# Kernel optimization log

Hardware: AMD Instinct MI355X
Metric: run time of the kernel (lower is better)

The kernel has to match this reference:

```python
import jax, jax.numpy as jnp
import numpy as np

B, T, D, H, K = 8, 512, 768, 8, 4
HD = D // H
SCALE = 1.0 / float(np.sqrt(HD))
EPS = 1e-5


def _ln(x, g, b):
    m = jnp.mean(x, -1, keepdims=True)
    v = jnp.mean((x - m) ** 2, -1, keepdims=True)
    return (x - m) * jax.lax.rsqrt(v + EPS) * g + b


def _attn(q, k, v, mask=None):
    # q,k,v: [B,T,D] -> multi-head scaled dot product, returns [B,T,D]
    sp = lambda t: t.reshape(B, T, H, HD).transpose(0, 2, 1, 3)  # [B,H,T,hd]
    a = jnp.einsum('bhqd,bhkd->bhqk', sp(q), sp(k)) * SCALE
    if mask is not None:
        a = jnp.where(mask, -jnp.inf, a)
    a = jax.nn.softmax(a, -1)
    o = jnp.einsum('bhqk,bhkd->bhqd', a, sp(v))
    return o.transpose(0, 2, 1, 3).reshape(B, T, D)


def setup_inputs() -> dict:
    key = jax.random.key(0)
    ks = iter(jax.random.split(key, 20))
    n = lambda shp: jax.random.normal(next(ks), shp, jnp.float32) * 0.02
    z = lambda shp: jnp.zeros(shp, jnp.float32)
    o = lambda shp: jnp.ones(shp, jnp.float32)
    return dict(
        x=jax.random.normal(next(ks), (B, T, D), jnp.float32),
        router_w1=n((128, D)), router_b1=z((128,)),
        router_w2=n((2 * K, 128)), router_b2=z((2 * K,)),
        norm_s_g=o((D,)), norm_s_b=z((D,)),
        norm_t_g=o((D,)), norm_t_b=z((D,)),
        norm_mlp_g=o((D,)), norm_mlp_b=z((D,)),
        sp_wqkv=n((K, 3 * D, D)), sp_bqkv=z((K, 3 * D)),
        sp_wo=n((K, D, D)), sp_bo=z((K, D)),
        tp_wq=n((K, D, D)), tp_bq=z((K, D)),
        tp_wk=n((K, D, D)), tp_bk=z((K, D)),
        tp_wv=n((K, D, D)), tp_bv=z((K, D)),
        tp_wo=n((K, D, D)), tp_bo=z((K, D)),
        cross_wqkv=n((3 * D, D)), cross_bqkv=z((3 * D,)),
        cross_wo=n((D, D)), cross_bo=z((D,)),
        mlp_w1=n((4 * D, D)), mlp_b1=z((4 * D,)),
        mlp_w2=n((D, 4 * D)), mlp_b2=z((D,)),
    )


def _forward(x, router_w1, router_b1, router_w2, router_b2,
             norm_s_g, norm_s_b, norm_t_g, norm_t_b, norm_mlp_g, norm_mlp_b,
             sp_wqkv, sp_bqkv, sp_wo, sp_bo,
             tp_wq, tp_bq, tp_wk, tp_bk, tp_wv, tp_bv, tp_wo, tp_bo,
             cross_wqkv, cross_bqkv, cross_wo, cross_bo,
             mlp_w1, mlp_b1, mlp_w2, mlp_b2):
    # --- router: top-1 expert per sample for each branch ---
    h = jax.nn.gelu(x.mean(1) @ router_w1.T + router_b1, approximate=False)
    route = jax.nn.softmax(h @ router_w2.T + router_b2, -1)  # [B, 2K]
    idx_s = jnp.argmax(route[:, :K], -1)  # [B] top-1 spatial expert
    idx_t = jnp.argmax(route[:, K:], -1)  # [B] top-1 temporal expert

    # --- spatial branch: per-sample routed MultiheadAttention (self-attn) ---
    xn = _ln(x, norm_s_g, norm_s_b)
    qkv = jnp.einsum('btd,bed->bte', xn, sp_wqkv[idx_s]) + sp_bqkv[idx_s][:, None, :]
    q, k, v = jnp.split(qkv, 3, -1)
    so = _attn(q, k, v)
    spatial_out = jnp.einsum('btd,bed->bte', so, sp_wo[idx_s]) + sp_bo[idx_s][:, None, :]

    # --- temporal branch: per-sample routed causal attention (with residual) ---
    xt = _ln(x, norm_t_g, norm_t_b)
    qt = jnp.einsum('btd,bed->bte', xt, tp_wq[idx_t]) + tp_bq[idx_t][:, None, :]
    kt = jnp.einsum('btd,bed->bte', xt, tp_wk[idx_t]) + tp_bk[idx_t][:, None, :]
    vt = jnp.einsum('btd,bed->bte', xt, tp_wv[idx_t]) + tp_bv[idx_t][:, None, :]
    causal = jnp.triu(jnp.ones((T, T), bool), 1)
    to = _attn(qt, kt, vt, mask=causal)
    to = jnp.einsum('btd,bed->bte', to, tp_wo[idx_t]) + tp_bo[idx_t][:, None, :]
    temporal_out = xt + to  # CausalTimeAttention2 adds residual to its (normed) query

    # --- cross attention fusing the two branches ---
    cq = spatial_out @ cross_wqkv[:D].T + cross_bqkv[:D]
    ck = temporal_out @ cross_wqkv[D:2 * D].T + cross_bqkv[D:2 * D]
    cv = temporal_out @ cross_wqkv[2 * D:].T + cross_bqkv[2 * D:]
    fused = _attn(cq, ck, cv) @ cross_wo.T + cross_bo

    x = x + fused
    y = jax.nn.gelu(_ln(x, norm_mlp_g, norm_mlp_b) @ mlp_w1.T + mlp_b1, approximate=False)
    x = x + (y @ mlp_w2.T + mlp_b2)
    return x


def reference(x, router_w1, router_b1, router_w2, router_b2,
              norm_s_g, norm_s_b, norm_t_g, norm_t_b, norm_mlp_g, norm_mlp_b,
              sp_wqkv, sp_bqkv, sp_wo, sp_bo,
              tp_wq, tp_bq, tp_wk, tp_bk, tp_wv, tp_bv, tp_wo, tp_bo,
              cross_wqkv, cross_bqkv, cross_wo, cross_bo,
              mlp_w1, mlp_b1, mlp_w2, mlp_b2):
    return _forward(x, router_w1, router_b1, router_w2, router_b2,
                    norm_s_g, norm_s_b, norm_t_g, norm_t_b, norm_mlp_g, norm_mlp_b,
                    sp_wqkv, sp_bqkv, sp_wo, sp_bo,
                    tp_wq, tp_bq, tp_wk, tp_bk, tp_wv, tp_bv, tp_wo, tp_bo,
                    cross_wqkv, cross_bqkv, cross_wo, cross_bo,
                    mlp_w1, mlp_b1, mlp_w2, mlp_b2)
```

## Files before the change

### kernel.cpp

```cpp
#include <hip/hip_runtime.h>
#include <math.h>

#define BB 8
#define TT 512
#define DD 768
#define HH 8
#define HDIM 96
#define DDDD 589824LL

typedef short s16x8 __attribute__((ext_vector_type(8)));
typedef float f32x4 __attribute__((ext_vector_type(4)));
typedef unsigned short u16;

__device__ inline unsigned short f2bf(float f) {
    union { float f; unsigned u; } v; v.f = f;
    unsigned u = v.u;
    unsigned r = (u + 0x7fffu + ((u >> 16) & 1u)) >> 16;
    return (unsigned short)r;
}

__device__ inline float bf2f(u16 h) {
    union { unsigned u; float f; } v; v.u = ((unsigned)h) << 16; return v.f;
}

__device__ inline float gelu_exact(float x) {
    return 0.5f * x * (1.0f + erff(x * 0.70710678118654752440f));
}

__device__ __forceinline__ void gload16(const void* g, void* l) {
    __builtin_amdgcn_global_load_lds(
        (const __attribute__((address_space(1))) unsigned int*)g,
        (__attribute__((address_space(3))) unsigned int*)l,
        16, 0, 0);
}

__device__ __forceinline__ long long tix(int m, int k, int ldn) {
    return ((long long)(m >> 6) * (ldn >> 3) + (k >> 3)) * 512 + ((m & 63) << 3) + (k & 7);
}

#define CUM1  7077888LL
#define CUM2  9437184LL
#define CUM5  16515072LL
#define CUM6  18874368LL
#define CUM7  20643840LL
#define CUM8  21233664LL
#define CUM9  23592960LL
#define CUM10 25952256LL

__global__ __launch_bounds__(256) void cvt_kernel(
    const float* __restrict__ s0, const float* __restrict__ s1,
    const float* __restrict__ s2, const float* __restrict__ s3,
    const float* __restrict__ s4, const float* __restrict__ s5,
    const float* __restrict__ s6, const float* __restrict__ s7,
    const float* __restrict__ s8, const float* __restrict__ s9,
    u16* __restrict__ dpool)
{
    int t = blockIdx.x;
    const float* sa = nullptr; const float* sb = nullptr; const float* sc = nullptr;
    long long dbase; int K = 768; int tpmode = 0;
    if (t < 864) {
        int e = t / 216; t -= e * 216;
        sa = s0 + (long long)e * 2304 * 768; dbase = e * 3 * DDDD;
    } else if (t < 1152) {
        t -= 864; int e = t / 72; t -= e * 72;
        sa = s1 + (long long)e * DDDD; dbase = CUM1 + e * DDDD;
    } else if (t < 2016) {
        t -= 1152; int e = t / 216; t -= e * 216; tpmode = 1;
        sa = s2 + (long long)e * DDDD; sb = s3 + (long long)e * DDDD;
        sc = s4 + (long long)e * DDDD; dbase = CUM2 + e * 3 * DDDD;
    } else if (t < 2304) {
        t -= 2016; int e = t / 72; t -= e * 72;
        sa = s5 + (long long)e * DDDD; dbase = CUM5 + e * DDDD;
    } else if (t < 2520) {
        t -= 2304; sa = s6; dbase = CUM6;
    } else if (t < 2592) {
        t -= 2520; sa = s7; dbase = CUM7;
    } else if (t < 2880) {
        t -= 2592; sa = s8; dbase = CUM8;
    } else {
        t -= 2880; sa = s9; dbase = CUM9; K = 3072;
    }
    int tiles_k = K >> 6;
    int nt = t / tiles_k, kb = t - nt * tiles_k;
    int n0 = nt * 128, k0 = kb * 64;

    __shared__ u16 lds[8256];

    int tid = threadIdx.x;
    #pragma unroll
    for (int it = 0; it < 4; ++it) {
        int sl = tid + it * 256;
        int r = sl >> 3, kw = sl & 7;
        int n = n0 + r;
        const float* src;
        if (tpmode) {
            if (n < 768)       src = sa + (long long)n * 768;
            else if (n < 1536) src = sb + (long long)(n - 768) * 768;
            else               src = sc + (long long)(n - 1536) * 768;
            src += k0 + kw * 8;
        } else {
            src = sa + (long long)n * K + k0 + kw * 8;
        }
        float4 a = *(const float4*)src;
        float4 b = *(const float4*)(src + 4);
        s16x8 o;
        o[0] = f2bf(a.x); o[1] = f2bf(a.y); o[2] = f2bf(a.z); o[3] = f2bf(a.w);
        o[4] = f2bf(b.x); o[5] = f2bf(b.y); o[6] = f2bf(b.z); o[7] = f2bf(b.w);
        *(s16x8*)&lds[(kw * 129 + r) * 8] = o;
    }
    __syncthreads();
    long long dbase2 = dbase + ((long long)nt * (K >> 3) + (long long)kb * 8) * 1024;
    #pragma unroll
    for (int it = 0; it < 4; ++it) {
        int sl = tid + it * 256;
        int kw = sl >> 7, r = sl & 127;
        *(s16x8*)(dpool + dbase2 + (long long)sl * 8) = *(const s16x8*)&lds[(kw * 129 + r) * 8];
    }
}

__global__ __launch_bounds__(256) void pack_tpb_kernel(
    const float* __restrict__ bq, const float* __restrict__ bk,
    const float* __restrict__ bv, float* __restrict__ dst)
{
    int t = blockIdx.x * 256 + threadIdx.x;
    if (t >= 4 * 2304) return;
    int e = t / 2304, n = t - e * 2304;
    float v = (n < 768) ? bq[e * 768 + n]
            : (n < 1536) ? bk[e * 768 + n - 768]
            : bv[e * 768 + n - 1536];
    dst[t] = v;
}

#define SLABB 4096

template<int OUT_MODE, int RES_MODE>
__global__ __launch_bounds__(256) void gemm_bf16_kernel(
    const u16* __restrict__ A, long long sAb,
    const u16* __restrict__ B, const int* __restrict__ bidx, long long sBexp,
    void* __restrict__ Cv, long long sCb, int ldc,
    const float* __restrict__ bias, long long sBiasExp,
    const void* __restrict__ residv, long long sResB, int ldr,
    int act, int N, int K)
{
    int nbx = gridDim.x, nby = gridDim.y;
    int nblk = nbx * nby * (int)gridDim.z;
    int lin = blockIdx.x + nbx * (blockIdx.y + nby * blockIdx.z);
    int q = nblk >> 3, r = nblk & 7;
    int xcd = lin & 7, pos = lin >> 3;
    int nl = (xcd < r ? xcd * (q + 1) : r * (q + 1) + (xcd - r) * q) + pos;
    int bx = nl % nbx; int t1 = nl / nbx; int by = t1 % nby; int bz = t1 / nby;

    int zb = bz;
    int kw8 = K >> 3;
    const u16* Ab = A + zb * sAb + (long long)by * kw8 * 512;
    const u16* Bb = B + (bidx ? (long long)bidx[zb] * sBexp : 0)
                      + (long long)bx * kw8 * 1024;
    const float* biasb = bias ? (bias + (bidx ? (long long)bidx[zb] * sBiasExp : 0)) : nullptr;

    __shared__ __align__(16) u16 Bs[6][SLABB];

    int tid = threadIdx.x;
    int wave = tid >> 6, lane = tid & 63;
    int wr = wave >> 1, wc = wave & 1;
    int lrow = lane & 15, lkg = lane >> 4;

    f32x4 acc[2][4];
    #pragma unroll
    for (int i = 0; i < 2; i++)
        #pragma unroll
        for (int j = 0; j < 4; j++)
            acc[i][j] = (f32x4){0.f, 0.f, 0.f, 0.f};

    long long aoff0 = (long long)lkg * 512 + (wr * 32 + 0 * 16 + lrow) * 8;
    long long aoff1 = (long long)lkg * 512 + (wr * 32 + 1 * 16 + lrow) * 8;

    const u16* bgt = Bb + tid * 8;
    u16* bl0 = (u16*)Bs + tid * 8;
    u16* bl1 = (u16*)Bs + (tid + 256) * 8;

    s16x8 abuf[3][2];

    int nK = K >> 5;

    gload16(bgt,            bl0);
    gload16(bgt + 2048,     bl1);
    gload16(bgt + SLABB,        bl0 + SLABB);
    gload16(bgt + SLABB + 2048, bl1 + SLABB);
    gload16(bgt + 2 * SLABB,        bl0 + 2 * SLABB);
    gload16(bgt + 2 * SLABB + 2048, bl1 + 2 * SLABB);
    abuf[0][0] = *(const s16x8*)(Ab + aoff0);
    abuf[0][1] = *(const s16x8*)(Ab + aoff1);
    gload16(bgt + 3 * SLABB,        bl0 + 3 * SLABB);
    gload16(bgt + 3 * SLABB + 2048, bl1 + 3 * SLABB);
    abuf[1][0] = *(const s16x8*)(Ab + 2048 + aoff0);
    abuf[1][1] = *(const s16x8*)(Ab + 2048 + aoff1);
    gload16(bgt + 4 * SLABB,        bl0 + 4 * SLABB);
    gload16(bgt + 4 * SLABB + 2048, bl1 + 4 * SLABB);

    for (int ktb = 0; ktb < nK; ktb += 6) {
        #pragma unroll
        for (int u = 0; u < 6; ++u) {
            int kt = ktb + u;
            if (kt + 6 <= nK) asm volatile("s_waitcnt vmcnt(6)" ::: "memory");
            else              asm volatile("s_waitcnt vmcnt(0)" ::: "memory");
            __builtin_amdgcn_s_barrier();
            __builtin_amdgcn_sched_barrier(0);

            if (kt + 2 < nK) {
                const u16* ap = Ab + (long long)(kt + 2) * 2048;
                abuf[(u + 2) % 3][0] = *(const s16x8*)(ap + aoff0);
                abuf[(u + 2) % 3][1] = *(const s16x8*)(ap + aoff1);
            }
            if (kt + 5 < nK) {
                const u16* bp = bgt + (long long)(kt + 5) * SLABB;
                int sl = (u + 5) % 6;
                gload16(bp,        bl0 + sl * SLABB);
                gload16(bp + 2048, bl1 + sl * SLABB);
            }

            const u16* Bsb = &Bs[u][0];
            s16x8 bf[4];
            #pragma unroll
            for (int j = 0; j < 4; ++j)
                bf[j] = *(const s16x8*)&Bsb[(lkg * 128 + wc * 64 + j * 16 + lrow) * 8];
            #pragma unroll
            for (int i = 0; i < 2; ++i)
                #pragma unroll
                for (int j = 0; j < 4; ++j)
                    acc[i][j] = __builtin_amdgcn_mfma_f32_16x16x32_bf16(abuf[u % 3][i], bf[j], acc[i][j], 0, 0, 0);
        }
    }

    int n0 = bx * 128;
    int m0 = by * 64;
    float* Cf = (float*)Cv + zb * sCb;
    u16* Ch = (u16*)Cv + zb * sCb;
    const float* Rf = (const float*)residv + zb * sResB;
    const u16* Rh = (const u16*)residv + zb * sResB;
    int col16 = lane & 15;
    int rq = (lane >> 4) * 4;
    #pragma unroll
    for (int j = 0; j < 4; ++j) {
        int n = n0 + wc * 64 + j * 16 + col16;
        float bv = biasb ? biasb[n] : 0.0f;
        #pragma unroll
        for (int i = 0; i < 2; ++i) {
            #pragma unroll
            for (int r2 = 0; r2 < 4; ++r2) {
                int m = m0 + wr * 32 + i * 16 + rq + r2;
                float v = acc[i][j][r2] + bv;
                if (act == 1) v = gelu_exact(v);
                if (RES_MODE == 1) v += Rf[(long long)m * ldr + n];
                if (RES_MODE == 2) v += bf2f(Rh[tix(m, n, ldr)]);
                if (OUT_MODE == 0) Cf[(long long)m * ldc + n] = v;
                if (OUT_MODE == 1) Ch[(long long)m * ldc + n] = f2bf(v);
                if (OUT_MODE == 2) Ch[tix(m, n, ldc)] = f2bf(v);
            }
        }
    }
}

__global__ __launch_bounds__(256, 2) void attn_kernel(
    const u16* __restrict__ QKV, u16* __restrict__ Out,
    int causal, float scale)
{
    int qt = blockIdx.x;
    int bh = blockIdx.y;
    int b = bh >> 3;
    int h = bh & 7;
    const u16* Qb = QKV + (long long)b * TT * 3 * DD + (long long)h * HDIM;
    const u16* Kb = Qb + DD;
    const u16* Vb = Qb + 2 * DD;
    u16* Ob = Out + (long long)b * TT * DD;

    __shared__ __align__(16) u16 Qs[64 * 104];
    __shared__ __align__(16) u16 Ks[64 * 104];
    __shared__ __align__(16) u16 Vs[96 * 72];
    __shared__ __align__(16) u16 Ps[64 * 72];

    int tid = threadIdx.x;
    int wave = tid >> 6;
    int lane = tid & 63;
    int col16 = lane & 15;
    int lkg = lane >> 4;
    int lk = lkg * 8;
    int m0 = qt * 64;

    #pragma unroll
    for (int it = 0; it < 3; ++it) {
        int s = tid + it * 256;
        int r = s / 12, c8 = (s % 12) * 8;
        *(s16x8*)&Qs[r * 104 + c8] = *(const s16x8*)(Qb + (long long)(m0 + r) * (3 * DD) + c8);
    }
    __syncthreads();

    s16x8 qf[3];
    #pragma unroll
    for (int kk = 0; kk < 3; ++kk)
        qf[kk] = *(const s16x8*)&Qs[(wave * 16 + col16) * 104 + kk * 32 + lk];

    f32x4 acc[32];
    #pragma unroll
    for (int n = 0; n < 32; ++n) acc[n] = (f32x4){0.f, 0.f, 0.f, 0.f};

    #pragma unroll
    for (int kt = 0; kt < 8; ++kt) {
        #pragma unroll
        for (int it = 0; it < 3; ++it) {
            int s = tid + it * 256;
            int r = s / 12, c8 = (s % 12) * 8;
            *(s16x8*)&Ks[r * 104 + c8] = *(const s16x8*)(Kb + (long long)(kt * 64 + r) * (3 * DD) + c8);
        }
        __syncthreads();
        #pragma unroll
        for (int kk = 0; kk < 3; ++kk) {
            #pragma unroll
            for (int j = 0; j < 4; ++j) {
                s16x8 bfr = *(const s16x8*)&Ks[(j * 16 + col16) * 104 + kk * 32 + lk];
                acc[kt * 4 + j] = __builtin_amdgcn_mfma_f32_16x16x32_bf16(qf[kk], bfr, acc[kt * 4 + j], 0, 0, 0);
            }
        }
        __syncthreads();
    }

    int rowbase = m0 + wave * 16 + lkg * 4;
    float mx[4];
    #pragma unroll
    for (int r = 0; r < 4; ++r) mx[r] = -3.0e38f;
    #pragma unroll
    for (int n = 0; n < 32; ++n) {
        int colg = n * 16 + col16;
        #pragma unroll
        for (int r = 0; r < 4; ++r) {
            float v = acc[n][r] * scale;
            if (causal && colg > rowbase + r) v = -3.0e38f;
            acc[n][r] = v;
            mx[r] = fmaxf(mx[r], v);
        }
    }
    #pragma unroll
    for (int m = 1; m <= 8; m <<= 1)
        #pragma unroll
        for (int r = 0; r < 4; ++r)
            mx[r] = fmaxf(mx[r], __shfl_xor(mx[r], m, 64));

    float sum[4] = {0.f, 0.f, 0.f, 0.f};
    #pragma unroll
    for (int n = 0; n < 32; ++n) {
        #pragma unroll
        for (int r = 0; r < 4; ++r) {
            float e = __expf(acc[n][r] - mx[r]);
            acc[n][r] = e;
            sum[r] += e;
        }
    }
    #pragma unroll
    for (int m = 1; m <= 8; m <<= 1)
        #pragma unroll
        for (int r = 0; r < 4; ++r)
            sum[r] += __shfl_xor(sum[r], m, 64);
    float inv[4];
    #pragma unroll
    for (int r = 0; r < 4; ++r) inv[r] = 1.0f / sum[r];

    f32x4 oacc[6];
    #pragma unroll
    for (int j = 0; j < 6; ++j) oacc[j] = (f32x4){0.f, 0.f, 0.f, 0.f};

    #pragma unroll
    for (int kt = 0; kt < 8; ++kt) {
        __syncthreads();
        #pragma unroll
        for (int j = 0; j < 4; ++j) {
            #pragma unroll
            for (int r = 0; r < 4; ++r)
                Ps[(wave * 16 + lkg * 4 + r) * 72 + j * 16 + col16] = f2bf(acc[kt * 4 + j][r]);
        }
        #pragma unroll
        for (int it = 0; it < 3; ++it) {
            int s = tid + it * 256;
            int key = s / 12, c8 = (s % 12) * 8;
            s16x8 v = *(const s16x8*)(Vb + (long long)(kt * 64 + key) * (3 * DD) + c8);
            #pragma unroll
            for (int e = 0; e < 8; ++e)
                Vs[(c8 + e) * 72 + key] = (u16)v[e];
        }
        __syncthreads();
        #pragma unroll
        for (int kk = 0; kk < 2; ++kk) {
            s16x8 pf = *(const s16x8*)&Ps[(wave * 16 + col16) * 72 + kk * 32 + lk];
            #pragma unroll
            for (int j = 0; j < 6; ++j) {
                s16x8 vf = *(const s16x8*)&Vs[(j * 16 + col16) * 72 + kk * 32 + lk];
                oacc[j] = __builtin_amdgcn_mfma_f32_16x16x32_bf16(pf, vf, oacc[j], 0, 0, 0);
            }
        }
    }

    int rquad = lkg * 4;
    #pragma unroll
    for (int j = 0; j < 6; ++j) {
        int d = h * 96 + j * 16 + col16;
        #pragma unroll
        for (int r = 0; r < 4; ++r) {
            int row = m0 + wave * 16 + rquad + r;
            Ob[tix(row, d, DD)] = f2bf(oacc[j][r] * inv[r]);
        }
    }
}

__global__ __launch_bounds__(256) void ln_kernel(
    const float* __restrict__ x, const float* __restrict__ g,
    const float* __restrict__ b, u16* __restrict__ out)
{
    long long row = blockIdx.x;
    const float* xr = x + row * DD;
    u16* ob = out + (row >> 9) * ((long long)TT * DD);
    int m = (int)(row & 511);
    int t = threadIdx.x;
    float vals[3];
    float s = 0.f, ss = 0.f;
    #pragma unroll
    for (int i = 0; i < 3; i++) {
        float v = xr[t + i * 256];
        vals[i] = v; s += v; ss += v * v;
    }
    __shared__ float rs[256], rss[256];
    rs[t] = s; rss[t] = ss; __syncthreads();
    for (int k = 128; k > 0; k >>= 1) {
        if (t < k) { rs[t] += rs[t + k]; rss[t] += rss[t + k]; }
        __syncthreads();
    }
    float mean = rs[0] * (1.0f / DD);
    float var = rss[0] * (1.0f / DD) - mean * mean;
    float inv = rsqrtf(var + 1e-5f);
    #pragma unroll
    for (int i = 0; i < 3; i++) {
        int d = t + i * 256;
        ob[tix(m, d, DD)] = f2bf((vals[i] - mean) * inv * g[d] + b[d]);
    }
}

__global__ __launch_bounds__(256) void mean_part_kernel(
    const float* __restrict__ x, float* __restrict__ part)
{
    int b = blockIdx.x, dseg = blockIdx.y, rc = blockIdx.z;
    int d = dseg * 256 + threadIdx.x;
    const float* xb = x + (long long)b * TT * DD;
    float s = 0.f;
    int r0 = rc * 64;
    for (int r = r0; r < r0 + 64; ++r) s += xb[(long long)r * DD + d];
    part[((long long)b * 8 + rc) * DD + d] = s;
}

__global__ __launch_bounds__(128) void router_kernel(
    const float* __restrict__ part, const float* __restrict__ w1,
    const float* __restrict__ b1, const float* __restrict__ w2,
    const float* __restrict__ b2, int* __restrict__ idx)
{
    int b = blockIdx.x, t = threadIdx.x;
    __shared__ float xm[DD];
    __shared__ float h[128];
    __shared__ float logits[8];
    for (int i = t; i < DD; i += 128) {
        float s = 0.f;
        for (int rc = 0; rc < 8; ++rc) s += part[((long long)b * 8 + rc) * DD + i];
        xm[i] = s * (1.0f / TT);
    }
    __syncthreads();
    {
        float s = b1[t];
        const float* w = w1 + (long long)t * DD;
        for (int d = 0; d < DD; ++d) s += xm[d] * w[d];
        h[t] = gelu_exact(s);
    }
    __syncthreads();
    if (t < 8) {
        float s = b2[t];
        const float* w = w2 + t * 128;
        for (int d = 0; d < 128; ++d) s += h[d] * w[d];
        logits[t] = s;
    }
    __syncthreads();
    if (t == 0) {
        int bsix = 0;
        for (int i = 1; i < 4; i++) if (logits[i] > logits[bsix]) bsix = i;
        int btix = 4;
        for (int i = 5; i < 8; i++) if (logits[i] > logits[btix]) btix = i;
        idx[b] = bsix;
        idx[b + BB] = btix - 4;
    }
}

static void run_gemm2(hipStream_t stream,
    const u16* A, long long sAb,
    const u16* B, const int* bidx, long long sBexp,
    void* C, long long sCb, int ldc,
    const float* bias, long long sBiasExp,
    const void* resid, long long sResB, int ldr,
    int act, int N, int K, int outmode, int resmode)
{
    dim3 grid(N / 128, 8, BB);
    if (outmode == 1)
        gemm_bf16_kernel<1, 0><<<grid, 256, 0, stream>>>(A, sAb, B, bidx, sBexp,
            C, sCb, ldc, bias, sBiasExp, resid, sResB, ldr, act, N, K);
    else if (outmode == 2 && resmode == 0)
        gemm_bf16_kernel<2, 0><<<grid, 256, 0, stream>>>(A, sAb, B, bidx, sBexp,
            C, sCb, ldc, bias, sBiasExp, resid, sResB, ldr, act, N, K);
    else if (outmode == 2)
        gemm_bf16_kernel<2, 2><<<grid, 256, 0, stream>>>(A, sAb, B, bidx, sBexp,
            C, sCb, ldc, bias, sBiasExp, resid, sResB, ldr, act, N, K);
    else
        gemm_bf16_kernel<0, 1><<<grid, 256, 0, stream>>>(A, sAb, B, bidx, sBexp,
            C, sCb, ldc, bias, sBiasExp, resid, sResB, ldr, act, N, K);
}

extern "C" void kernel_launch(void* const* d_in, const int* in_sizes, int n_in,
                              void* d_out, int out_size, void* d_ws, size_t ws_size,
                              hipStream_t stream)
{
    const float* x       = (const float*)d_in[0];
    const float* rw1     = (const float*)d_in[1];
    const float* rb1     = (const float*)d_in[2];
    const float* rw2     = (const float*)d_in[3];
    const float* rb2     = (const float*)d_in[4];
    const float* gs      = (const float*)d_in[5];
    const float* bs      = (const float*)d_in[6];
    const float* gt      = (const float*)d_in[7];
    const float* btt     = (const float*)d_in[8];
    const float* gm      = (const float*)d_in[9];
    const float* bm      = (const float*)d_in[10];
    const float* sp_wqkv = (const float*)d_in[11];
    const float* sp_bqkv = (const float*)d_in[12];
    const float* sp_wo   = (const float*)d_in[13];
    const float* sp_bo   = (const float*)d_in[14];
    const float* tp_wq   = (const float*)d_in[15];
    const float* tp_bq   = (const float*)d_in[16];
    const float* tp_wk   = (const float*)d_in[17];
    const float* tp_bk   = (const float*)d_in[18];
    const float* tp_wv   = (const float*)d_in[19];
    const float* tp_bv   = (const float*)d_in[20];
    const float* tp_wo   = (const float*)d_in[21];
    const float* tp_bo   = (const float*)d_in[22];
    const float* c_wqkv  = (const float*)d_in[23];
    const float* c_bqkv  = (const float*)d_in[24];
    const float* c_wo    = (const float*)d_in[25];
    const float* c_bo    = (const float*)d_in[26];
    const float* m_w1    = (const float*)d_in[27];
    const float* m_b1    = (const float*)d_in[28];
    const float* m_w2    = (const float*)d_in[29];
    const float* m_b2    = (const float*)d_in[30];
    float* out = (float*)d_out;

    float* ws = (float*)d_ws;
    size_t o = 0;
    float* part  = ws + o; o += (size_t)BB * 8 * DD;
    int*   idx   = (int*)(ws + o); o += 16;
    float* tpb   = ws + o; o += 4 * 2304;
    float* x1b   = ws + o; o += (size_t)4096 * DD;
    u16* xnb   = (u16*)(ws + o); o += (size_t)4096 * DD / 2;
    u16* tmp1b = (u16*)(ws + o); o += (size_t)4096 * DD / 2;
    u16* tmp2b = (u16*)(ws + o); o += (size_t)4096 * DD / 2;
    u16* soutb = (u16*)(ws + o); o += (size_t)4096 * DD / 2;
    u16* toutb = (u16*)(ws + o); o += (size_t)4096 * DD / 2;
    u16* qkvb  = (u16*)(ws + o); o += (size_t)4096 * 2304 / 2;
    u16* yb    = (u16*)(ws + o); o += (size_t)4096 * 3072 / 2;
    u16* wpool = (u16*)(ws + o); o += (size_t)CUM10 / 2;

    u16* w_sp_qkv = wpool;
    u16* w_sp_wo  = wpool + CUM1;
    u16* w_tp_qkv = wpool + CUM2;
    u16* w_tp_o   = wpool + CUM5;
    u16* w_c_qkv  = wpool + CUM6;
    u16* w_c_wo   = wpool + CUM7;
    u16* w_m1     = wpool + CUM8;
    u16* w_m2     = wpool + CUM9;

    int* idx_s = idx;
    int* idx_t = idx + BB;

    const long long sTD  = (long long)TT * DD;
    const long long sT3D = (long long)TT * 3 * DD;
    const long long sT4D = (long long)TT * 4 * DD;
    const float qk_scale = 1.0f / sqrtf((float)HDIM);

    cvt_kernel<<<3168, 256, 0, stream>>>(
        sp_wqkv, sp_wo, tp_wq, tp_wk, tp_wv, tp_wo, c_wqkv, c_wo, m_w1, m_w2, wpool);
    pack_tpb_kernel<<<36, 256, 0, stream>>>(tp_bq, tp_bk, tp_bv, tpb);

    mean_part_kernel<<<dim3(BB, 3, 8), 256, 0, stream>>>(x, part);
    router_kernel<<<BB, 128, 0, stream>>>(part, rw1, rb1, rw2, rb2, idx);

    ln_kernel<<<4096, 256, 0, stream>>>(x, gs, bs, xnb);
    run_gemm2(stream, xnb, sTD, w_sp_qkv, idx_s, 3 * DDDD,
              qkvb, sT3D, 3 * DD, sp_bqkv, 3 * DD, nullptr, 0, 0,
              0, 3 * DD, DD, 1, 0);
    attn_kernel<<<dim3(TT / 64, BB * HH), 256, 0, stream>>>(qkvb, tmp1b, 0, qk_scale);
    run_gemm2(stream, tmp1b, sTD, w_sp_wo, idx_s, DDDD,
              soutb, sTD, DD, sp_bo, DD, nullptr, 0, 0,
              0, DD, DD, 2, 0);

    ln_kernel<<<4096, 256, 0, stream>>>(x, gt, btt, xnb);
    run_gemm2(stream, xnb, sTD, w_tp_qkv, idx_t, 3 * DDDD,
              qkvb, sT3D, 3 * DD, tpb, 3 * DD, nullptr, 0, 0,
              0, 3 * DD, DD, 1, 0);
    attn_kernel<<<dim3(TT / 64, BB * HH), 256, 0, stream>>>(qkvb, tmp1b, 1, qk_scale);
    run_gemm2(stream, tmp1b, sTD, w_tp_o, idx_t, DDDD,
              toutb, sTD, DD, tp_bo, DD, xnb, sTD, DD,
              0, DD, DD, 2, 2);

    run_gemm2(stream, soutb, sTD, w_c_qkv, nullptr, 0,
              qkvb, sT3D, 3 * DD, c_bqkv, 0, nullptr, 0, 0,
              0, DD, DD, 1, 0);
    run_gemm2(stream, toutb, sTD, w_c_qkv + DDDD, nullptr, 0,
              qkvb + DD, sT3D, 3 * DD, c_bqkv + DD, 0, nullptr, 0, 0,
              0, 2 * DD, DD, 1, 0);
    attn_kernel<<<dim3(TT / 64, BB * HH), 256, 0, stream>>>(qkvb, tmp1b, 0, qk_scale);
    run_gemm2(stream, tmp1b, sTD, w_c_wo, nullptr, 0,
              x1b, sTD, DD, c_bo, 0, x, sTD, DD,
              0, DD, DD, 0, 1);

    ln_kernel<<<4096, 256, 0, stream>>>(x1b, gm, bm, tmp2b);
    run_gemm2(stream, tmp2b, sTD, w_m1, nullptr, 0,
              yb, sT4D, 4 * DD, m_b1, 0, nullptr, 0, 0,
              1, 4 * DD, DD, 2, 0);
    run_gemm2(stream, yb, sT4D, w_m2, nullptr, 0,
              out, sTD, DD, m_b2, 0, x1b, sTD, DD,
              0, DD, 4 * DD, 0, 1);
}
```

Before: 613.3 us.

## Batch spatial and temporal branches into shared GEMM, attention and LN launches

Result: no change. 618.6 us (+0.9%).

```diff
diff --git a/kernel.cpp b/kernel.cpp
--- a/kernel.cpp
+++ b/kernel.cpp
@@ -133,14 +133,16 @@
 
 #define SLABB 4096
 
-template<int OUT_MODE, int RES_MODE>
-__global__ __launch_bounds__(256) void gemm_bf16_kernel(
-    const u16* __restrict__ A, long long sAb,
-    const u16* __restrict__ B, const int* __restrict__ bidx, long long sBexp,
-    void* __restrict__ Cv, long long sCb, int ldc,
-    const float* __restrict__ bias, long long sBiasExp,
-    const void* __restrict__ residv, long long sResB, int ldr,
-    int act, int N, int K)
+struct GA {
+    const u16* A; long long sAb;
+    const u16* B; const int* bidx; long long sBexp;
+    void* C; long long sCb; int ldc;
+    const float* bias; long long sBiasExp;
+    const void* resid; long long sResB; int ldr;
+    int act; int N; int K; int om; int rm;
+};
+
+__global__ __launch_bounds__(256) void gemm_u_kernel(GA g0, GA g1)
 {
     int nbx = gridDim.x, nby = gridDim.y;
     int nblk = nbx * nby * (int)gridDim.z;
@@ -150,12 +152,15 @@
     int nl = (xcd < r ? xcd * (q + 1) : r * (q + 1) + (xcd - r) * q) + pos;
     int bx = nl % nbx; int t1 = nl / nbx; int by = t1 % nby; int bz = t1 / nby;
 
-    int zb = bz;
-    int kw8 = K >> 3;
-    const u16* Ab = A + zb * sAb + (long long)by * kw8 * 512;
-    const u16* Bb = B + (bidx ? (long long)bidx[zb] * sBexp : 0)
-                      + (long long)bx * kw8 * 1024;
-    const float* biasb = bias ? (bias + (bidx ? (long long)bidx[zb] * sBiasExp : 0)) : nullptr;
+    const GA g = (bz >= 8) ? g1 : g0;
+    int zb = bz & 7;
+    if (bx * 128 >= g.N) return;
+
+    int kw8 = g.K >> 3;
+    const u16* Ab = g.A + zb * g.sAb + (long long)by * kw8 * 512;
+    const u16* Bb = g.B + (g.bidx ? (long long)g.bidx[zb] * g.sBexp : 0)
+                        + (long long)bx * kw8 * 1024;
+    const float* biasb = g.bias + (g.bidx ? (long long)g.bidx[zb] * g.sBiasExp : 0);
 
     __shared__ __align__(16) u16 Bs[6][SLABB];
 
@@ -180,7 +185,7 @@
 
     s16x8 abuf[3][2];
 
-    int nK = K >> 5;
+    int nK = g.K >> 5;
 
     gload16(bgt,            bl0);
     gload16(bgt + 2048,     bl1);
@@ -233,39 +238,44 @@
 
     int n0 = bx * 128;
     int m0 = by * 64;
-    float* Cf = (float*)Cv + zb * sCb;
-    u16* Ch = (u16*)Cv + zb * sCb;
-    const float* Rf = (const float*)residv + zb * sResB;
-    const u16* Rh = (const u16*)residv + zb * sResB;
+    float* Cf = (float*)g.C + zb * g.sCb;
+    u16* Ch = (u16*)g.C + zb * g.sCb;
+    const float* Rf = (const float*)g.resid + zb * g.sResB;
+    const u16* Rh = (const u16*)g.resid + zb * g.sResB;
     int col16 = lane & 15;
     int rq = (lane >> 4) * 4;
     #pragma unroll
     for (int j = 0; j < 4; ++j) {
         int n = n0 + wc * 64 + j * 16 + col16;
-        float bv = biasb ? biasb[n] : 0.0f;
+        float bv = biasb[n];
         #pragma unroll
         for (int i = 0; i < 2; ++i) {
             #pragma unroll
             for (int r2 = 0; r2 < 4; ++r2) {
                 int m = m0 + wr * 32 + i * 16 + rq + r2;
                 float v = acc[i][j][r2] + bv;
-                if (act == 1) v = gelu_exact(v);
-                if (RES_MODE == 1) v += Rf[(long long)m * ldr + n];
-                if (RES_MODE == 2) v += bf2f(Rh[tix(m, n, ldr)]);
-                if (OUT_MODE == 0) Cf[(long long)m * ldc + n] = v;
-                if (OUT_MODE == 1) Ch[(long long)m * ldc + n] = f2bf(v);
-                if (OUT_MODE == 2) Ch[tix(m, n, ldc)] = f2bf(v);
+                if (g.act == 1) v = gelu_exact(v);
+                if (g.rm == 1) v += Rf[(long long)m * g.ldr + n];
+                else if (g.rm == 2) v += bf2f(Rh[tix(m, n, g.ldr)]);
+                if (g.om == 0)      Cf[(long long)m * g.ldc + n] = v;
+                else if (g.om == 1) Ch[(long long)m * g.ldc + n] = f2bf(v);
+                else                Ch[tix(m, n, g.ldc)] = f2bf(v);
             }
         }
     }
 }
 
 __global__ __launch_bounds__(256, 2) void attn_kernel(
-    const u16* __restrict__ QKV, u16* __restrict__ Out,
-    int causal, float scale)
+    const u16* __restrict__ QKV0, u16* __restrict__ Out0, int causal0,
+    const u16* __restrict__ QKV1, u16* __restrict__ Out1, int causal1,
+    float scale)
 {
     int qt = blockIdx.x;
-    int bh = blockIdx.y;
+    int set = blockIdx.y >> 6;
+    int bh = blockIdx.y & 63;
+    const u16* QKV = set ? QKV1 : QKV0;
+    u16* Out = set ? Out1 : Out0;
+    int causal = set ? causal1 : causal0;
     int b = bh >> 3;
     int h = bh & 7;
     const u16* Qb = QKV + (long long)b * TT * 3 * DD + (long long)h * HDIM;
@@ -406,6 +416,43 @@
             int row = m0 + wave * 16 + rquad + r;
             Ob[tix(row, d, DD)] = f2bf(oacc[j][r] * inv[r]);
         }
+    }
+}
+
+__global__ __launch_bounds__(256) void ln2_kernel(
+    const float* __restrict__ x,
+    const float* __restrict__ g0, const float* __restrict__ b0, u16* __restrict__ out0,
+    const float* __restrict__ g1, const float* __restrict__ b1, u16* __restrict__ out1)
+{
+    int set = blockIdx.x >> 12;
+    long long row = blockIdx.x & 4095;
+    const float* g = set ? g1 : g0;
+    const float* b = set ? b1 : b0;
+    u16* out = set ? out1 : out0;
+    const float* xr = x + row * DD;
+    u16* ob = out + (row >> 9) * ((long long)TT * DD);
+    int m = (int)(row & 511);
+    int t = threadIdx.x;
+    float vals[3];
+    float s = 0.f, ss = 0.f;
+    #pragma unroll
+    for (int i = 0; i < 3; i++) {
+        float v = xr[t + i * 256];
+        vals[i] = v; s += v; ss += v * v;
+    }
+    __shared__ float rs[256], rss[256];
+    rs[t] = s; rss[t] = ss; __syncthreads();
+    for (int k = 128; k > 0; k >>= 1) {
+        if (t < k) { rs[t] += rs[t + k]; rss[t] += rss[t + k]; }
+        __syncthreads();
+    }
+    float mean = rs[0] * (1.0f / DD);
+    float var = rss[0] * (1.0f / DD) - mean * mean;
+    float inv = rsqrtf(var + 1e-5f);
+    #pragma unroll
+    for (int i = 0; i < 3; i++) {
+        int d = t + i * 256;
+        ob[tix(m, d, DD)] = f2bf((vals[i] - mean) * inv * g[d] + b[d]);
     }
 }
 
@@ -490,29 +537,6 @@
         idx[b] = bsix;
         idx[b + BB] = btix - 4;
     }
-}
-
-static void run_gemm2(hipStream_t stream,
-    const u16* A, long long sAb,
-    const u16* B, const int* bidx, long long sBexp,
-    void* C, long long sCb, int ldc,
-    const float* bias, long long sBiasExp,
-    const void* resid, long long sResB, int ldr,
-    int act, int N, int K, int outmode, int resmode)
-{
-    dim3 grid(N / 128, 8, BB);
-    if (outmode == 1)
-        gemm_bf16_kernel<1, 0><<<grid, 256, 0, stream>>>(A, sAb, B, bidx, sBexp,
-            C, sCb, ldc, bias, sBiasExp, resid, sResB, ldr, act, N, K);
-    else if (outmode == 2 && resmode == 0)
-        gemm_bf16_kernel<2, 0><<<grid, 256, 0, stream>>>(A, sAb, B, bidx, sBexp,
-            C, sCb, ldc, bias, sBiasExp, resid, sResB, ldr, act, N, K);
-    else if (outmode == 2)
-        gemm_bf16_kernel<2, 2><<<grid, 256, 0, stream>>>(A, sAb, B, bidx, sBexp,
-            C, sCb, ldc, bias, sBiasExp, resid, sResB, ldr, act, N, K);
-    else
-        gemm_bf16_kernel<0, 1><<<grid, 256, 0, stream>>>(A, sAb, B, bidx, sBexp,
-            C, sCb, ldc, bias, sBiasExp, resid, sResB, ldr, act, N, K);
 }
 
 extern "C" void kernel_launch(void* const* d_in, const int* in_sizes, int n_in,
@@ -558,14 +582,18 @@
     int*   idx   = (int*)(ws + o); o += 16;
     float* tpb   = ws + o; o += 4 * 2304;
     float* x1b   = ws + o; o += (size_t)4096 * DD;
-    u16* xnb   = (u16*)(ws + o); o += (size_t)4096 * DD / 2;
-    u16* tmp1b = (u16*)(ws + o); o += (size_t)4096 * DD / 2;
+    u16* xnb_s = (u16*)(ws + o); o += (size_t)4096 * DD / 2;
+    u16* tmp1s = (u16*)(ws + o); o += (size_t)4096 * DD / 2;
+    u16* tmp1t = (u16*)(ws + o); o += (size_t)4096 * DD / 2;
     u16* tmp2b = (u16*)(ws + o); o += (size_t)4096 * DD / 2;
     u16* soutb = (u16*)(ws + o); o += (size_t)4096 * DD / 2;
     u16* toutb = (u16*)(ws + o); o += (size_t)4096 * DD / 2;
-    u16* qkvb  = (u16*)(ws + o); o += (size_t)4096 * 2304 / 2;
+    u16* qkvb_s = (u16*)(ws + o); o += (size_t)4096 * 2304 / 2;
     u16* yb    = (u16*)(ws + o); o += (size_t)4096 * 3072 / 2;
     u16* wpool = (u16*)(ws + o); o += (size_t)CUM10 / 2;
+
+    u16* xnb_t  = tmp2b;
+    u16* qkvb_t = yb;
 
     u16* w_sp_qkv = wpool;
     u16* w_sp_wo  = wpool + CUM1;
@@ -591,40 +619,40 @@
     mean_part_kernel<<<dim3(BB, 3, 8), 256, 0, stream>>>(x, part);
     router_kernel<<<BB, 128, 0, stream>>>(part, rw1, rb1, rw2, rb2, idx);
 
-    ln_kernel<<<4096, 256, 0, stream>>>(x, gs, bs, xnb);
-    run_gemm2(stream, xnb, sTD, w_sp_qkv, idx_s, 3 * DDDD,
-              qkvb, sT3D, 3 * DD, sp_bqkv, 3 * DD, nullptr, 0, 0,
-              0, 3 * DD, DD, 1, 0);
-    attn_kernel<<<dim3(TT / 64, BB * HH), 256, 0, stream>>>(qkvb, tmp1b, 0, qk_scale);
-    run_gemm2(stream, tmp1b, sTD, w_sp_wo, idx_s, DDDD,
-              soutb, sTD, DD, sp_bo, DD, nullptr, 0, 0,
-              0, DD, DD, 2, 0);
-
-    ln_kernel<<<4096, 256, 0, stream>>>(x, gt, btt, xnb);
-    run_gemm2(stream, xnb, sTD, w_tp_qkv, idx_t, 3 * DDDD,
-              qkvb, sT3D, 3 * DD, tpb, 3 * DD, nullptr, 0, 0,
-              0, 3 * DD, DD, 1, 0);
-    attn_kernel<<<dim3(TT / 64, BB * HH), 256, 0, stream>>>(qkvb, tmp1b, 1, qk_scale);
-    run_gemm2(stream, tmp1b, sTD, w_tp_o, idx_t, DDDD,
-              toutb, sTD, DD, tp_bo, DD, xnb, sTD, DD,
-              0, DD, DD, 2, 2);
-
-    run_gemm2(stream, soutb, sTD, w_c_qkv, nullptr, 0,
-              qkvb, sT3D, 3 * DD, c_bqkv, 0, nullptr, 0, 0,
-              0, DD, DD, 1, 0);
-    run_gemm2(stream, toutb, sTD, w_c_qkv + DDDD, nullptr, 0,
-              qkvb + DD, sT3D, 3 * DD, c_bqkv + DD, 0, nullptr, 0, 0,
-              0, 2 * DD, DD, 1, 0);
-    attn_kernel<<<dim3(TT / 64, BB * HH), 256, 0, stream>>>(qkvb, tmp1b, 0, qk_scale);
-    run_gemm2(stream, tmp1b, sTD, w_c_wo, nullptr, 0,
-              x1b, sTD, DD, c_bo, 0, x, sTD, DD,
-              0, DD, DD, 0, 1);
+    ln2_kernel<<<8192, 256, 0, stream>>>(x, gs, bs, xnb_s, gt, btt, xnb_t);
+
+    GA q0 = {xnb_s, sTD, w_sp_qkv, idx_s, 3 * DDDD, qkvb_s, sT3D, 3 * DD,
+             sp_bqkv, 3 * DD, nullptr, 0, 0, 0, 3 * DD, DD, 1, 0};
+    GA q1 = {xnb_t, sTD, w_tp_qkv, idx_t, 3 * DDDD, qkvb_t, sT3D, 3 * DD,
+             tpb, 3 * DD, nullptr, 0, 0, 0, 3 * DD, DD, 1, 0};
+    gemm_u_kernel<<<dim3(18, 8, 16), 256, 0, stream>>>(q0, q1);
+
+    attn_kernel<<<dim3(8, 128), 256, 0, stream>>>(
+        qkvb_s, tmp1s, 0, qkvb_t, tmp1t, 1, qk_scale);
+
+    GA w0 = {tmp1s, sTD, w_sp_wo, idx_s, DDDD, soutb, sTD, DD,
+             sp_bo, DD, nullptr, 0, 0, 0, DD, DD, 2, 0};
+    GA w1 = {tmp1t, sTD, w_tp_o, idx_t, DDDD, toutb, sTD, DD,
+             tp_bo, DD, xnb_t, sTD, DD, 0, DD, DD, 2, 2};
+    gemm_u_kernel<<<dim3(6, 8, 16), 256, 0, stream>>>(w0, w1);
+
+    GA c0 = {soutb, sTD, w_c_qkv, nullptr, 0, qkvb_s, sT3D, 3 * DD,
+             c_bqkv, 0, nullptr, 0, 0, 0, DD, DD, 1, 0};
+    GA c1 = {toutb, sTD, w_c_qkv + DDDD, nullptr, 0, qkvb_s + DD, sT3D, 3 * DD,
+             c_bqkv + DD, 0, nullptr, 0, 0, 0, 2 * DD, DD, 1, 0};
+    gemm_u_kernel<<<dim3(12, 8, 16), 256, 0, stream>>>(c0, c1);
+
+    attn_kernel<<<dim3(8, 64), 256, 0, stream>>>(
+        qkvb_s, tmp1s, 0, qkvb_s, tmp1s, 0, qk_scale);
+    GA cw = {tmp1s, sTD, w_c_wo, nullptr, 0, x1b, sTD, DD,
+             c_bo, 0, x, sTD, DD, 0, DD, DD, 0, 1};
+    gemm_u_kernel<<<dim3(6, 8, 8), 256, 0, stream>>>(cw, cw);
 
     ln_kernel<<<4096, 256, 0, stream>>>(x1b, gm, bm, tmp2b);
-    run_gemm2(stream, tmp2b, sTD, w_m1, nullptr, 0,
-              yb, sT4D, 4 * DD, m_b1, 0, nullptr, 0, 0,
-              1, 4 * DD, DD, 2, 0);
-    run_gemm2(stream, yb, sT4D, w_m2, nullptr, 0,
-              out, sTD, DD, m_b2, 0, x1b, sTD, DD,
-              0, DD, 4 * DD, 0, 1);
-}
+    GA m1 = {tmp2b, sTD, w_m1, nullptr, 0, yb, sT4D, 4 * DD,
+             m_b1, 0, nullptr, 0, 0, 1, 4 * DD, DD, 2, 0};
+    gemm_u_kernel<<<dim3(24, 8, 8), 256, 0, stream>>>(m1, m1);
+    GA m2 = {yb, sT4D, w_m2, nullptr, 0, out, sTD, DD,
+             m_b2, 0, x1b, sTD, DD, 0, DD, 4 * DD, 0, 1};
+    gemm_u_kernel<<<dim3(6, 8, 8), 256, 0, stream>>>(m2, m2);
+}
```
